# Optimization experiments

Hardware: AMD Instinct MI355X
Metric: run time of the kernel (lower is better)

The kernel has to match this reference:

```python
import jax, jax.numpy as jnp
import numpy as np

OUT_DIM = 1024


def setup_inputs() -> dict:
    key = jax.random.key(0)
    k1, k2, k3, k4 = jax.random.split(key, 4)
    B, N, D = 4, 2048, 1024
    s = 1.0 / np.sqrt(D)
    return {
        "x": jax.random.normal(k1, (B, N, D), dtype=jnp.float32),
        "W_query": jax.random.normal(k2, (D, OUT_DIM), dtype=jnp.float32) * s,
        "W_key": jax.random.normal(k3, (D, OUT_DIM), dtype=jnp.float32) * s,
        "W_value": jax.random.normal(k4, (D, OUT_DIM), dtype=jnp.float32) * s,
    }


def reference(x, W_query, W_key, W_value):
    # x: [B, N, D_in]; W_*: [D_in, D_out] (torch Linear weight transposed)
    q = jnp.einsum("bnd,de->bne", x, W_query)
    k = jnp.einsum("bnd,de->bne", x, W_key)
    v = jnp.einsum("bnd,de->bne", x, W_value)
    sqrt_d = jnp.sqrt(jnp.asarray(OUT_DIM, dtype=jnp.float32))
    scores = jnp.einsum("bie,bje->bij", q, k) / sqrt_d  # [B, N, N]
    # NOTE: original uses softmax over dim=1 (query axis), not the usual dim=2
    attn = jax.nn.softmax(scores, axis=1)
    # dropout with train=False is identity (eval-mode reference)
    # out = attn^T @ v  ->  out[b, j] = sum_i attn[b, i, j] * v[b, i]
    return jnp.einsum("bij,bie->bje", attn, v)
```

## Files before the change

kernel.cpp:

```cpp
#include <hip/hip_runtime.h>
#include <math.h>


typedef __bf16 bf16x8 __attribute__((ext_vector_type(8)));
typedef float f32x4 __attribute__((ext_vector_type(4)));

static __device__ __forceinline__ unsigned short f2bf(float f) {
    unsigned u = __float_as_uint(f);
    u += 0x7fff + ((u >> 16) & 1);
    return (unsigned short)(u >> 16);
}

#define GLDS16(gptr, lptr)                                                            \
    __builtin_amdgcn_global_load_lds(                                                 \
        (const __attribute__((address_space(1))) void*)(gptr),                        \
        (__attribute__((address_space(3))) void*)(lptr), 16, 0, 0)

#define BARSYNC  __builtin_amdgcn_s_barrier()
#define WAITLGKM do { asm volatile("s_waitcnt lgkmcnt(0)" ::: "memory");    \
                      __builtin_amdgcn_sched_barrier(0); } while (0)

__device__ __forceinline__ void gemm256_core(
    const unsigned short* __restrict__ Ab,
    const unsigned short* __restrict__ Bb,
    const long ld, unsigned short* lds, f32x4 acc[8][4])
{
    const int tid  = threadIdx.x;
    const int w    = tid >> 6;
    const int lane = tid & 63;

    const int r  = lane >> 3;
    const int s  = lane & 7;
    const int cg = (s ^ r) * 8;

    const int fr    = lane & 15;
    const int quad  = lane >> 4;
    const int sw    = fr & 7;
    const int arow0 = (w >> 2) * 128;
    const int brow0 = (w & 3) * 64;

#define STG_A(t, mh, buf) do {                                              \
    const int rb_ = (w >> 2) * 128 + (mh) * 64 + (w & 3) * 16;              \
    const unsigned short* g_ = Ab + (long)(rb_ + r) * ld + (long)(t) * 64 + cg; \
    unsigned short* d_ = lds + (buf) * 16384 + rb_ * 64;                    \
    GLDS16(g_, d_); GLDS16(g_ + 8 * ld, d_ + 512); } while (0)
#define STG_B(t, nh, buf) do {                                              \
    const int rb_ = (w >> 1) * 64 + (nh) * 32 + (w & 1) * 16;               \
    const unsigned short* g_ = Bb + (long)(rb_ + r) * ld + (long)(t) * 64 + cg; \
    unsigned short* d_ = lds + 32768 + (buf) * 16384 + rb_ * 64;            \
    GLDS16(g_, d_); GLDS16(g_ + 8 * ld, d_ + 512); } while (0)

    bf16x8 af[4][2], bfA[2][2], bfB[2][2];
#define LOADA(buf, mh) do {                                                 \
    _Pragma("unroll") for (int ks_ = 0; ks_ < 2; ks_++)                     \
    _Pragma("unroll") for (int i_ = 0; i_ < 4; i_++)                        \
        af[i_][ks_] = *(const bf16x8*)&lds[(buf) * 16384 +                  \
            (arow0 + (mh) * 64 + i_ * 16 + fr) * 64 +                       \
            ((ks_ * 4 + quad) ^ sw) * 8]; } while (0)
#define LOADB(BF, buf, nh) do {                                             \
    _Pragma("unroll") for (int ks_ = 0; ks_ < 2; ks_++)                     \
    _Pragma("unroll") for (int j_ = 0; j_ < 2; j_++)                        \
        BF[j_][ks_] = *(const bf16x8*)&lds[32768 + (buf) * 16384 +          \
            (brow0 + (nh) * 32 + j_ * 16 + fr) * 64 +                       \
            ((ks_ * 4 + quad) ^ sw) * 8]; } while (0)

#define MFMA16(mh, nh, BF) do {                                             \
    __builtin_amdgcn_s_setprio(1);                                          \
    _Pragma("unroll") for (int ks_ = 0; ks_ < 2; ks_++)                     \
    _Pragma("unroll") for (int i_ = 0; i_ < 4; i_++)                        \
    _Pragma("unroll") for (int j_ = 0; j_ < 2; j_++)                        \
        acc[(mh) * 4 + i_][(nh) * 2 + j_] =                                 \
            __builtin_amdgcn_mfma_f32_16x16x32_bf16(                        \
                af[i_][ks_], BF[j_][ks_],                                   \
                acc[(mh) * 4 + i_][(nh) * 2 + j_], 0, 0, 0);                \
    __builtin_amdgcn_s_setprio(0); } while (0)

#pragma unroll
    for (int i = 0; i < 8; i++)
#pragma unroll
        for (int j = 0; j < 4; j++) acc[i][j] = f32x4{0.f, 0.f, 0.f, 0.f};

    STG_A(0, 0, 0); STG_A(0, 1, 0); STG_B(0, 0, 0); STG_B(0, 1, 0);
    STG_A(1, 0, 1); STG_B(1, 1, 1);
    asm volatile("s_waitcnt vmcnt(4)" ::: "memory");
    BARSYNC;

#pragma unroll 1
    for (int i = 0; i < 8; ++i) {
        const int t1 = 2 * i + 1;
        const int t2 = (2 * i + 2) & 15;
        const int t3 = (2 * i + 3) & 15;
        LOADA(0, 0); LOADB(bfA, 0, 0); STG_B(t1, 0, 1);
        BARSYNC; WAITLGKM; MFMA16(0, 0, bfA); BARSYNC;
        LOADB(bfB, 0, 1); STG_A(t1, 1, 1);
        BARSYNC; WAITLGKM; MFMA16(0, 1, bfB); BARSYNC;
        LOADA(0, 1); STG_A(t2, 0, 0);
        BARSYNC; WAITLGKM; MFMA16(1, 1, bfB); BARSYNC;
        STG_B(t2, 1, 0);
        BARSYNC; MFMA16(1, 0, bfA);
        asm volatile("s_waitcnt vmcnt(4)" ::: "memory"); BARSYNC;
        LOADA(1, 0); LOADB(bfA, 1, 0); STG_A(t2, 1, 0);
        BARSYNC; WAITLGKM; MFMA16(0, 0, bfA); BARSYNC;
        LOADB(bfB, 1, 1); STG_B(t2, 0, 0);
        BARSYNC; WAITLGKM; MFMA16(0, 1, bfB); BARSYNC;
        LOADA(1, 1); STG_A(t3, 0, 1);
        BARSYNC; WAITLGKM; MFMA16(1, 1, bfB); BARSYNC;
        STG_B(t3, 1, 1);
        BARSYNC; MFMA16(1, 0, bfA);
        asm volatile("s_waitcnt vmcnt(4)" ::: "memory"); BARSYNC;
    }
    asm volatile("s_waitcnt vmcnt(0)" ::: "memory");

#undef STG_A
#undef STG_B
#undef LOADA
#undef LOADB
#undef MFMA16
}

__device__ __forceinline__ void gemm_v128_core(
    const unsigned short* __restrict__ Ab,
    const unsigned short* __restrict__ Bb,
    unsigned short* lds, f32x4 acc[4][4])
{
    const int tid  = threadIdx.x;
    const int w    = tid >> 6;
    const int lane = tid & 63;

    const int r  = lane >> 3;
    const int s  = lane & 7;
    const int cg = (s ^ r) * 8;

    const int fr    = lane & 15;
    const int quad  = lane >> 4;
    const int sw    = fr & 7;
    const int arow0 = (w >> 2) * 64;
    const int brow0 = (w & 3) * 64;

#define STG_VA(t, mh, buf) do {                                             \
    const int rb_ = (w >> 2) * 64 + (mh) * 32 + (w & 3) * 8;                \
    const unsigned short* g_ = Ab + (long)(rb_ + r) * 1024 + (long)(t) * 64 + cg; \
    unsigned short* d_ = lds + (buf) * 8192 + rb_ * 64;                     \
    GLDS16(g_, d_); } while (0)
#define STG_VB(t, nh, buf) do {                                             \
    const int rb_ = (w >> 1) * 64 + (nh) * 32 + (w & 1) * 16;               \
    const unsigned short* g_ = Bb + (long)(rb_ + r) * 1024 + (long)(t) * 64 + cg; \
    unsigned short* d_ = lds + 16384 + (buf) * 16384 + rb_ * 64;            \
    GLDS16(g_, d_); GLDS16(g_ + 8 * 1024, d_ + 512); } while (0)

    bf16x8 af[2][2], bfA[2][2], bfB[2][2];
#define LOADVA(buf, mh) do {                                                \
    _Pragma("unroll") for (int ks_ = 0; ks_ < 2; ks_++)                     \
    _Pragma("unroll") for (int i_ = 0; i_ < 2; i_++)                        \
        af[i_][ks_] = *(const bf16x8*)&lds[(buf) * 8192 +                   \
            (arow0 + (mh) * 32 + i_ * 16 + fr) * 64 +                       \
            ((ks_ * 4 + quad) ^ sw) * 8]; } while (0)
#define LOADVB(BF, buf, nh) do {                                            \
    _Pragma("unroll") for (int ks_ = 0; ks_ < 2; ks_++)                     \
    _Pragma("unroll") for (int j_ = 0; j_ < 2; j_++)                        \
        BF[j_][ks_] = *(const bf16x8*)&lds[16384 + (buf) * 16384 +          \
            (brow0 + (nh) * 32 + j_ * 16 + fr) * 64 +                       \
            ((ks_ * 4 + quad) ^ sw) * 8]; } while (0)

#define MFMA_V(mh, nh, BF) do {                                             \
    __builtin_amdgcn_s_setprio(1);                                          \
    _Pragma("unroll") for (int ks_ = 0; ks_ < 2; ks_++)                     \
    _Pragma("unroll") for (int i_ = 0; i_ < 2; i_++)                        \
    _Pragma("unroll") for (int j_ = 0; j_ < 2; j_++)                        \
        acc[(mh) * 2 + i_][(nh) * 2 + j_] =                                 \
            __builtin_amdgcn_mfma_f32_16x16x32_bf16(                        \
                af[i_][ks_], BF[j_][ks_],                                   \
                acc[(mh) * 2 + i_][(nh) * 2 + j_], 0, 0, 0);                \
    __builtin_amdgcn_s_setprio(0); } while (0)

#pragma unroll
    for (int i = 0; i < 4; i++)
#pragma unroll
        for (int j = 0; j < 4; j++) acc[i][j] = f32x4{0.f, 0.f, 0.f, 0.f};

    STG_VA(0, 0, 0); STG_VA(0, 1, 0); STG_VB(0, 0, 0); STG_VB(0, 1, 0);
    STG_VA(1, 0, 1); STG_VB(1, 1, 1);
    asm volatile("s_waitcnt vmcnt(3)" ::: "memory");
    BARSYNC;

#pragma unroll 1
    for (int i = 0; i < 8; ++i) {
        const int t1 = 2 * i + 1;
        const int t2 = (2 * i + 2) & 15;
        const int t3 = (2 * i + 3) & 15;
        LOADVA(0, 0); LOADVB(bfA, 0, 0); STG_VB(t1, 0, 1);
        BARSYNC; WAITLGKM; MFMA_V(0, 0, bfA); BARSYNC;
        LOADVB(bfB, 0, 1); STG_VA(t1, 1, 1);
        BARSYNC; WAITLGKM; MFMA_V(0, 1, bfB); BARSYNC;
        LOADVA(0, 1); STG_VA(t2, 0, 0);
        BARSYNC; WAITLGKM; MFMA_V(1, 1, bfB); BARSYNC;
        STG_VB(t2, 1, 0);
        BARSYNC; MFMA_V(1, 0, bfA);
        asm volatile("s_waitcnt vmcnt(3)" ::: "memory"); BARSYNC;
        LOADVA(1, 0); LOADVB(bfA, 1, 0); STG_VA(t2, 1, 0);
        BARSYNC; WAITLGKM; MFMA_V(0, 0, bfA); BARSYNC;
        LOADVB(bfB, 1, 1); STG_VB(t2, 0, 0);
        BARSYNC; WAITLGKM; MFMA_V(0, 1, bfB); BARSYNC;
        LOADVA(1, 1); STG_VA(t3, 0, 1);
        BARSYNC; WAITLGKM; MFMA_V(1, 1, bfB); BARSYNC;
        STG_VB(t3, 1, 1);
        BARSYNC; MFMA_V(1, 0, bfA);
        asm volatile("s_waitcnt vmcnt(3)" ::: "memory"); BARSYNC;
    }
    asm volatile("s_waitcnt vmcnt(0)" ::: "memory");

#undef STG_VA
#undef STG_VB
#undef LOADVA
#undef LOADVB
#undef MFMA_V
}

__device__ __forceinline__ void pv256_core(
    const unsigned short* __restrict__ Ab,
    const unsigned short* __restrict__ Bb,
    unsigned short* lds, f32x4 acc[8][2])
{
    const int tid  = threadIdx.x;
    const int w    = tid >> 6;
    const int lane = tid & 63;

    const int r  = lane >> 3;
    const int s  = lane & 7;
    const int cg = (s ^ r) * 8;

    const int fr    = lane & 15;
    const int quad  = lane >> 4;
    const int sw    = fr & 7;
    const int arow0 = (w >> 2) * 128;
    const int brow0 = (w & 3) * 32;

#define STG_PA(t, mh, buf) do {                                             \
    const int rb_ = (w >> 2) * 128 + (mh) * 64 + (w & 3) * 16;              \
    const unsigned short* g_ = Ab + (long)(rb_ + r) * 2048 + (long)(t) * 64 + cg; \
    unsigned short* d_ = lds + (buf) * 16384 + rb_ * 64;                    \
    GLDS16(g_, d_); GLDS16(g_ + 8 * 2048, d_ + 512); } while (0)
#define STG_PB(t, nh, buf) do {                                             \
    const int rb_ = (w & 3) * 32 + (nh) * 16 + (w >> 2) * 8;                \
    const unsigned short* g_ = Bb + (long)(rb_ + r) * 8192 + (long)(t) * 64 + cg; \
    unsigned short* d_ = lds + 32768 + (buf) * 8192 + rb_ * 64;             \
    GLDS16(g_, d_); } while (0)

    bf16x8 af[4][2], bfA[2], bfB[2];
#define LOADPA(buf, mh) do {                                                \
    _Pragma("unroll") for (int ks_ = 0; ks_ < 2; ks_++)                     \
    _Pragma("unroll") for (int i_ = 0; i_ < 4; i_++)                        \
        af[i_][ks_] = *(const bf16x8*)&lds[(buf) * 16384 +                  \
            (arow0 + (mh) * 64 + i_ * 16 + fr) * 64 +                       \
            ((ks_ * 4 + quad) ^ sw) * 8]; } while (0)
#define LOADPB(BF, buf, nh) do {                                            \
    _Pragma("unroll") for (int ks_ = 0; ks_ < 2; ks_++)                     \
        BF[ks_] = *(const bf16x8*)&lds[32768 + (buf) * 8192 +               \
            (brow0 + (nh) * 16 + fr) * 64 +                                 \
            ((ks_ * 4 + quad) ^ sw) * 8]; } while (0)

#define MFMA8(mh, nh, BF) do {                                              \
    __builtin_amdgcn_s_setprio(1);                                          \
    _Pragma("unroll") for (int ks_ = 0; ks_ < 2; ks_++)                     \
    _Pragma("unroll") for (int i_ = 0; i_ < 4; i_++)                        \
        acc[(mh) * 4 + i_][nh] = __builtin_amdgcn_mfma_f32_16x16x32_bf16(   \
            af[i_][ks_], BF[ks_], acc[(mh) * 4 + i_][nh], 0, 0, 0);         \
    __builtin_amdgcn_s_setprio(0); } while (0)

#pragma unroll
    for (int i = 0; i < 8; i++)
#pragma unroll
        for (int j = 0; j < 2; j++) acc[i][j] = f32x4{0.f, 0.f, 0.f, 0.f};

    STG_PA(0, 0, 0); STG_PA(0, 1, 0); STG_PB(0, 0, 0); STG_PB(0, 1, 0);
    STG_PA(1, 0, 1); STG_PB(1, 1, 1);
    asm volatile("s_waitcnt vmcnt(3)" ::: "memory");
    BARSYNC;

#pragma unroll 1
    for (int i = 0; i < 16; ++i) {
        const int t1 = 2 * i + 1;
        const int t2 = (2 * i + 2) & 31;
        const int t3 = (2 * i + 3) & 31;
        LOADPA(0, 0); LOADPB(bfA, 0, 0); STG_PB(t1, 0, 1);
        BARSYNC; WAITLGKM; MFMA8(0, 0, bfA); BARSYNC;
        LOADPB(bfB, 0, 1); STG_PA(t1, 1, 1);
        BARSYNC; WAITLGKM; MFMA8(0, 1, bfB); BARSYNC;
        LOADPA(0, 1); STG_PA(t2, 0, 0);
        BARSYNC; WAITLGKM; MFMA8(1, 1, bfB); BARSYNC;
        STG_PB(t2, 1, 0);
        BARSYNC; MFMA8(1, 0, bfA);
        asm volatile("s_waitcnt vmcnt(3)" ::: "memory"); BARSYNC;
        LOADPA(1, 0); LOADPB(bfA, 1, 0); STG_PA(t2, 1, 0);
        BARSYNC; WAITLGKM; MFMA8(0, 0, bfA); BARSYNC;
        LOADPB(bfB, 1, 1); STG_PB(t2, 0, 0);
        BARSYNC; WAITLGKM; MFMA8(0, 1, bfB); BARSYNC;
        LOADPA(1, 1); STG_PA(t3, 0, 1);
        BARSYNC; WAITLGKM; MFMA8(1, 1, bfB); BARSYNC;
        STG_PB(t3, 1, 1);
        BARSYNC; MFMA8(1, 0, bfA);
        asm volatile("s_waitcnt vmcnt(3)" ::: "memory"); BARSYNC;
    }
    asm volatile("s_waitcnt vmcnt(0)" ::: "memory");

#undef STG_PA
#undef STG_PB
#undef LOADPA
#undef LOADPB
#undef MFMA8
}

__global__ __launch_bounds__(512, 2) void gemm_qk256(
    const unsigned short* __restrict__ A, const unsigned short* __restrict__ B,
    unsigned short* __restrict__ QK)
{
    __shared__ unsigned short lds[65536];
    const int orig = blockIdx.x;
    const int xcd  = orig & 7;
    const int pos  = orig >> 3;
    const long gm0 = (long)(xcd * 4 + (pos & 3)) * 256;
    const long gn0 = (long)(pos >> 2) * 256;

    f32x4 acc[8][4];
    gemm256_core(A + gm0 * 1024, B + gn0 * 1024, 1024, lds, acc);

    const int tid = threadIdx.x;
    const int w = tid >> 6, lane = tid & 63;
    const int fr = lane & 15, quad = lane >> 4;
    const int wm = (w >> 2) * 128, wn = (w & 3) * 64;

#pragma unroll
    for (int mi = 0; mi < 8; mi++) {
        const long rb = gm0 + wm + (mi >> 2) * 64 + (mi & 3) * 16 + quad * 4;
#pragma unroll
        for (int n = 0; n < 4; n++) {
            const long cb = gn0 + wn + n * 16 + fr;
#pragma unroll
            for (int rr = 0; rr < 4; rr++)
                QK[(rb + rr) * 2048L + cb] = f2bf(acc[mi][n][rr]);
        }
    }
}

__global__ __launch_bounds__(512, 2) void gemm_v128(
    const unsigned short* __restrict__ A, const unsigned short* __restrict__ B,
    unsigned short* __restrict__ Vt)
{
    __shared__ unsigned short lds[49152];
    const int orig = blockIdx.x;
    const int xcd  = orig & 7;
    const int pos  = orig >> 3;
    const long gm0 = (long)(xcd * 8 + (pos & 7)) * 128;
    const long gn0 = (long)(pos >> 3) * 256;

    f32x4 acc[4][4];
    gemm_v128_core(A + gm0 * 1024, B + gn0 * 1024, lds, acc);

    const int tid = threadIdx.x;
    const int w = tid >> 6, lane = tid & 63;
    const int fr = lane & 15, quad = lane >> 4;
    const int wm = (w >> 2) * 64, wn = (w & 3) * 64;

#pragma unroll
    for (int ai = 0; ai < 4; ai++) {
        const long rb = gm0 + wm + ai * 16 + quad * 4;
#pragma unroll
        for (int aj = 0; aj < 4; aj++) {
            const long ce = gn0 + wn + aj * 16 + fr;
            ushort4 o;
            o.x = f2bf(acc[ai][aj][0]);
            o.y = f2bf(acc[ai][aj][1]);
            o.z = f2bf(acc[ai][aj][2]);
            o.w = f2bf(acc[ai][aj][3]);
            *(ushort4*)&Vt[ce * 8192L + rb] = o;
        }
    }
}

__global__ __launch_bounds__(512, 2) void gemm_scores256(
    const unsigned short* __restrict__ QKb, unsigned short* __restrict__ P,
    float* __restrict__ l)
{
    __shared__ unsigned short lds[65536];
    const int orig = blockIdx.x;
    const int xcd  = orig & 7;
    const int pos  = orig >> 3;
    const int bz   = xcd >> 1;
    const long gm0 = (long)((xcd & 1) * 4 + (pos >> 3)) * 256;
    const long gn0 = (long)(pos & 7) * 256;

    const unsigned short* Ab = QKb + (long)bz * 2048 * 2048 + 1024 + gm0 * 2048;
    const unsigned short* Bb = QKb + (long)bz * 2048 * 2048 + gn0 * 2048;

    f32x4 acc[8][4];
    gemm256_core(Ab, Bb, 2048, lds, acc);

    const int tid = threadIdx.x;
    const int w = tid >> 6, lane = tid & 63;
    const int fr = lane & 15, quad = lane >> 4;
    const int wm = (w >> 2) * 128, wn = (w & 3) * 64;

    unsigned short* Pb = P + (long)bz * 2048 * 2048;
    float* lb = l + (long)bz * 2048;
    const float scale = 1.0f / 32.0f;
#pragma unroll
    for (int mi = 0; mi < 8; mi++) {
        const long rb = gm0 + wm + (mi >> 2) * 64 + (mi & 3) * 16 + quad * 4;
        float rs[4] = {0.f, 0.f, 0.f, 0.f};
#pragma unroll
        for (int n = 0; n < 4; n++) {
            const long cb = gn0 + wn + n * 16 + fr;
#pragma unroll
            for (int rr = 0; rr < 4; rr++) {
                float e = __expf(acc[mi][n][rr] * scale);
                rs[rr] += e;
                Pb[(rb + rr) * 2048L + cb] = f2bf(e);
            }
        }
#pragma unroll
        for (int rr = 0; rr < 4; rr++) {
#pragma unroll
            for (int m = 8; m > 0; m >>= 1) rs[rr] += __shfl_xor(rs[rr], m, 16);
        }
        if (fr == 0) {
#pragma unroll
            for (int rr = 0; rr < 4; rr++)
                atomicAdd(&lb[rb + rr], rs[rr]);
        }
    }
}

__global__ __launch_bounds__(512, 2) void gemm_pv256(
    const unsigned short* __restrict__ P, const unsigned short* __restrict__ Vt,
    const float* __restrict__ l, float* __restrict__ out)
{
    __shared__ unsigned short lds[49152];
    const int orig = blockIdx.x;
    const int xcd  = orig & 7;
    const int pos  = orig >> 3;
    const int bz   = xcd >> 1;
    const long gm0 = (long)((xcd & 1) * 4 + (pos >> 3)) * 256;
    const long gn0 = (long)(pos & 7) * 128;

    const unsigned short* Ab = P + (long)bz * 2048 * 2048 + gm0 * 2048;
    const unsigned short* Bb = Vt + gn0 * 8192 + (long)bz * 2048;

    f32x4 acc[8][2];
    pv256_core(Ab, Bb, lds, acc);

    const int tid = threadIdx.x;
    const int w = tid >> 6, lane = tid & 63;
    const int fr = lane & 15, quad = lane >> 4;
    const int wm = (w >> 2) * 128, wn = (w & 3) * 32;

    float* Ob = out + (long)bz * 2048 * 1024;
    const float* lb = l + (long)bz * 2048;
#pragma unroll
    for (int mi = 0; mi < 8; mi++) {
        const long rb = gm0 + wm + (mi >> 2) * 64 + (mi & 3) * 16 + quad * 4;
        float inv[4];
#pragma unroll
        for (int rr = 0; rr < 4; rr++) inv[rr] = 1.0f / lb[rb + rr];
#pragma unroll
        for (int nj = 0; nj < 2; nj++) {
            const long cb = gn0 + wn + nj * 16 + fr;
#pragma unroll
            for (int rr = 0; rr < 4; rr++)
                Ob[(rb + rr) * 1024L + cb] = acc[mi][nj][rr] * inv[rr];
        }
    }
}

__global__ __launch_bounds__(256) void prep(
    const float* __restrict__ x,
    const float* __restrict__ Wq, const float* __restrict__ Wk,
    const float* __restrict__ Wv,
    unsigned short* __restrict__ xb, unsigned short* __restrict__ Wqkvt,
    float* __restrict__ l)
{
    __shared__ float t[32][33];
    const int b = blockIdx.x;
    const int tid = threadIdx.x;
    if (b < 8192) {
        int i = b * 256 + tid;
        float4 v = ((const float4*)x)[i];
        ushort4 o;
        o.x = f2bf(v.x); o.y = f2bf(v.y); o.z = f2bf(v.z); o.w = f2bf(v.w);
        ((ushort4*)xb)[i] = o;
        return;
    }
    if (b == 8192 + 3072) {
        float4 z = {0.f, 0.f, 0.f, 0.f};
#pragma unroll
        for (int i = 0; i < 8; i++)
            ((float4*)l)[tid * 8 + i] = z;
        return;
    }
    int tix = b - 8192;
    const int w = tix >> 10;
    tix &= 1023;
    const float* W = (w == 0) ? Wq : (w == 1) ? Wk : Wv;
    unsigned short* Wt = Wqkvt + (long)w * 1024 * 1024;
    const int bx = (tix & 31) * 32;
    const int by = (tix >> 5) * 32;
    const int tx = tid & 31;
    const int ty = (tid >> 5) * 4;
#pragma unroll
    for (int j = 0; j < 4; j++)
        t[ty + j][tx] = W[(long)(by + ty + j) * 1024 + bx + tx];
    __syncthreads();
#pragma unroll
    for (int j = 0; j < 4; j++)
        Wt[(long)(bx + ty + j) * 1024 + by + tx] = f2bf(t[tx][ty + j]);
}

extern "C" void kernel_launch(void* const* d_in, const int* in_sizes, int n_in,
                              void* d_out, int out_size, void* d_ws,
                              size_t ws_size, hipStream_t stream)
{
    const float* x  = (const float*)d_in[0];
    const float* Wq = (const float*)d_in[1];
    const float* Wk = (const float*)d_in[2];
    const float* Wv = (const float*)d_in[3];
    float* out = (float*)d_out;

    const long M1 = 1024 * 1024;
    unsigned short* u     = (unsigned short*)d_ws;
    unsigned short* xb    = u;
    unsigned short* Wqkvt = u + 8 * M1;
    unsigned short* QKb   = Wqkvt + 3 * M1;
    unsigned short* Vtb   = QKb + 16 * M1;
    unsigned short* Pb    = Vtb + 8 * M1;
    float* l              = (float*)(Pb + 16 * M1);

    prep<<<dim3(8192 + 3072 + 1), dim3(256), 0, stream>>>(x, Wq, Wk, Wv, xb, Wqkvt, l);

    gemm_qk256<<<dim3(256), dim3(512), 0, stream>>>(xb, Wqkvt, QKb);

    gemm_v128<<<dim3(256), dim3(512), 0, stream>>>(xb, Wqkvt + 2 * M1, Vtb);

    gemm_scores256<<<dim3(256), dim3(512), 0, stream>>>(QKb, Pb, l);

    gemm_pv256<<<dim3(256), dim3(512), 0, stream>>>(Pb, Vtb, l, out);
}
```

Measured before the change: 221.0 us.

## Transpose QK and score GEMM outputs to enable vectorized 8-byte stores

The QK projection now swaps its operands so it writes the transposed result, and the scores GEMM swaps its A/B operand offsets and stores the exp tile transposed. Each lane can then pack four bf16 values into one ushort4 store instead of issuing four strided 2-byte stores. The softmax denominator is accumulated per column across the whole tile and reduced with two cross-quad shuffles, cutting the number of shuffles and atomics. The risk is that the transposed layout must stay consistent with the downstream PV kernel, whose code is not shown.

```diff
diff --git a/kernel.cpp b/kernel.cpp
--- a/kernel.cpp
+++ b/kernel.cpp
@@ -311,18 +311,18 @@
 }
 
 __global__ __launch_bounds__(512, 2) void gemm_qk256(
-    const unsigned short* __restrict__ A, const unsigned short* __restrict__ B,
+    const unsigned short* __restrict__ X, const unsigned short* __restrict__ W,
     unsigned short* __restrict__ QK)
 {
     __shared__ unsigned short lds[65536];
     const int orig = blockIdx.x;
     const int xcd  = orig & 7;
     const int pos  = orig >> 3;
-    const long gm0 = (long)(xcd * 4 + (pos & 3)) * 256;
-    const long gn0 = (long)(pos >> 2) * 256;
+    const long gm0 = (long)(pos >> 2) * 256;
+    const long gn0 = (long)(xcd * 4 + (pos & 3)) * 256;
 
     f32x4 acc[8][4];
-    gemm256_core(A + gm0 * 1024, B + gn0 * 1024, 1024, lds, acc);
+    gemm256_core(W + gm0 * 1024, X + gn0 * 1024, 1024, lds, acc);
 
     const int tid = threadIdx.x;
     const int w = tid >> 6, lane = tid & 63;
@@ -335,9 +335,12 @@
 #pragma unroll
         for (int n = 0; n < 4; n++) {
             const long cb = gn0 + wn + n * 16 + fr;
-#pragma unroll
-            for (int rr = 0; rr < 4; rr++)
-                QK[(rb + rr) * 2048L + cb] = f2bf(acc[mi][n][rr]);
+            ushort4 o;
+            o.x = f2bf(acc[mi][n][0]);
+            o.y = f2bf(acc[mi][n][1]);
+            o.z = f2bf(acc[mi][n][2]);
+            o.w = f2bf(acc[mi][n][3]);
+            *(ushort4*)&QK[cb * 2048L + rb] = o;
         }
     }
 }
@@ -389,8 +392,8 @@
     const long gm0 = (long)((xcd & 1) * 4 + (pos >> 3)) * 256;
     const long gn0 = (long)(pos & 7) * 256;
 
-    const unsigned short* Ab = QKb + (long)bz * 2048 * 2048 + 1024 + gm0 * 2048;
-    const unsigned short* Bb = QKb + (long)bz * 2048 * 2048 + gn0 * 2048;
+    const unsigned short* Ab = QKb + (long)bz * 2048 * 2048 + gm0 * 2048;
+    const unsigned short* Bb = QKb + (long)bz * 2048 * 2048 + 1024 + gn0 * 2048;
 
     f32x4 acc[8][4];
     gemm256_core(Ab, Bb, 2048, lds, acc);
@@ -403,30 +406,33 @@
     unsigned short* Pb = P + (long)bz * 2048 * 2048;
     float* lb = l + (long)bz * 2048;
     const float scale = 1.0f / 32.0f;
+
+    float colsum[4] = {0.f, 0.f, 0.f, 0.f};
 #pragma unroll
     for (int mi = 0; mi < 8; mi++) {
         const long rb = gm0 + wm + (mi >> 2) * 64 + (mi & 3) * 16 + quad * 4;
-        float rs[4] = {0.f, 0.f, 0.f, 0.f};
 #pragma unroll
         for (int n = 0; n < 4; n++) {
             const long cb = gn0 + wn + n * 16 + fr;
-#pragma unroll
-            for (int rr = 0; rr < 4; rr++) {
-                float e = __expf(acc[mi][n][rr] * scale);
-                rs[rr] += e;
-                Pb[(rb + rr) * 2048L + cb] = f2bf(e);
-            }
+            float e0 = __expf(acc[mi][n][0] * scale);
+            float e1 = __expf(acc[mi][n][1] * scale);
+            float e2 = __expf(acc[mi][n][2] * scale);
+            float e3 = __expf(acc[mi][n][3] * scale);
+            colsum[n] += (e0 + e1) + (e2 + e3);
+            ushort4 o;
+            o.x = f2bf(e0); o.y = f2bf(e1); o.z = f2bf(e2); o.w = f2bf(e3);
+            *(ushort4*)&Pb[cb * 2048L + rb] = o;
         }
-#pragma unroll
-        for (int rr = 0; rr < 4; rr++) {
-#pragma unroll
-            for (int m = 8; m > 0; m >>= 1) rs[rr] += __shfl_xor(rs[rr], m, 16);
-        }
-        if (fr == 0) {
-#pragma unroll
-            for (int rr = 0; rr < 4; rr++)
-                atomicAdd(&lb[rb + rr], rs[rr]);
-        }
+    }
+#pragma unroll
+    for (int n = 0; n < 4; n++) {
+        colsum[n] += __shfl_xor(colsum[n], 16);
+        colsum[n] += __shfl_xor(colsum[n], 32);
+    }
+    if (quad == 0) {
+#pragma unroll
+        for (int n = 0; n < 4; n++)
+            atomicAdd(&lb[gn0 + wn + n * 16 + fr], colsum[n]);
     }
 }
 
```

Result: no change. 217.2 us (-1.7%).
